# Performance work log

Measured on AMD Instinct MI355X. Metric: run time of the kernel, lower is better.

## Reference

```python
import jax, jax.numpy as jnp
import numpy as np

B, S, R, V, C, K, H = 256, 64, 256, 2000, 10, 6, 4
D = 256
DH = D // H
NEG = -1e9


def setup_inputs() -> dict:
    key = jax.random.key(0)
    ks = jax.random.split(key, 32)
    w = lambda i, shape: jax.random.normal(ks[i], shape, jnp.float32) * 0.05
    inp = {}
    inp["vis_emb"] = jax.random.normal(ks[0], (B * S, D), jnp.float32)
    # multi-hot concept vectors (sparse 0/1)
    inp["basic"] = (jax.random.uniform(ks[1], (R, V)) < 0.01).astype(jnp.float32)
    inp["crucial"] = (jax.random.uniform(ks[2], (R, V)) < 0.01).astype(jnp.float32)
    # to_b / to_k linears
    inp["Wtb"], inp["btb"] = w(3, (V, D)), w(4, (D,))
    inp["Wtk"], inp["btk"] = w(5, (V, D)), w(6, (D,))
    # cross attention (rule2vis): q/k/v/out projections
    inp["Wq"], inp["bq"] = w(7, (D, D)), w(8, (D,))
    inp["Wk"], inp["bk"] = w(9, (D, D)), w(10, (D,))
    inp["Wv"], inp["bv"] = w(11, (D, D)), w(12, (D,))
    inp["Wo"], inp["bo"] = w(13, (D, D)), w(14, (D,))
    # per-class GAT stacks: GAT(256->128), GAT(128->64), Linear(64->K)
    inp["W1"], inp["a1s"], inp["a1d"], inp["b1"] = w(15, (C, D, 128)), w(16, (C, 128)), w(17, (C, 128)), w(18, (C, 128))
    inp["W2"], inp["a2s"], inp["a2d"], inp["b2"] = w(19, (C, 128, 64)), w(20, (C, 64)), w(21, (C, 64)), w(22, (C, 64))
    inp["Wl"], inp["bl"] = w(23, (C, 64, K)), w(24, (C, K))
    # rule-graph adjacency: symmetric + self loops (PyG GATConv adds self loops)
    a0 = jax.random.uniform(ks[25], (R, R)) < 0.05
    inp["adj"] = a0 | a0.T | jnp.eye(R, dtype=bool)
    # class membership mask: each rule node belongs to one class head
    cls = jax.random.randint(ks[26], (R,), 0, C)
    inp["mask"] = (cls[None, :] == jnp.arange(C)[:, None]).astype(jnp.int32)
    return inp


def _gat(h, W, a_s, a_d, b, adj_bias):
    # h: [B,R,Fin] -> [B,R,Fout]; single-head PyG-style GATConv over dense adj
    hW = h @ W                                             # [B,R,F]
    e_dst = jnp.einsum('brf,f->br', hW, a_d)               # dst term
    e_src = jnp.einsum('brf,f->br', hW, a_s)               # src term
    e = jax.nn.leaky_relu(e_dst[:, :, None] + e_src[:, None, :], 0.2)  # [B,Rdst,Rsrc]
    alpha = jax.nn.softmax(e + adj_bias[None], axis=-1)
    return jnp.einsum('bij,bjf->bif', alpha, hW) + b


def reference(vis_emb, basic, crucial, Wtb, btb, Wtk, btk, Wq, bq, Wk, bk, Wv, bv,
              Wo, bo, W1, a1s, a1d, b1, W2, a2s, a2d, b2, Wl, bl, adj, mask):
    # rule embeddings: to_b(basic) + to_k(crucial)
    rule = basic @ Wtb + btb + crucial @ Wtk + btk         # [R,D]
    kv = vis_emb.reshape(B, S, D)
    q = jnp.broadcast_to(rule[None], (B, R, D))
    Q = (q @ Wq + bq).reshape(B, R, H, DH)
    Kx = (kv @ Wk + bk).reshape(B, S, H, DH)
    Vx = (kv @ Wv + bv).reshape(B, S, H, DH)
    att = jnp.einsum('brhd,bshd->bhrs', Q, Kx) / jnp.sqrt(jnp.float32(DH))
    att = jax.nn.softmax(att, axis=-1)
    emb = jnp.einsum('bhrs,bshd->brhd', att, Vx).reshape(B, R, D) @ Wo + bo  # [B,R,D]

    adj_bias = jnp.where(adj, 0.0, NEG).astype(emb.dtype)  # [R,R]
    outs = []
    for c in range(C):  # small fixed number of class heads
        h = emb * mask[c].astype(emb.dtype)[None, :, None]
        h = jax.nn.relu(_gat(h, W1[c], a1s[c], a1d[c], b1[c], adj_bias))
        h = _gat(h, W2[c], a2s[c], a2d[c], b2[c], adj_bias)  # dropout = eval identity
        h = h @ Wl[c] + bl[c]                                # [B,R,K]
        outs.append(jax.nn.log_softmax(h.sum(axis=1), axis=1))
    return jnp.stack(outs)  # [C,B,K]
```

## Files before the change

kernel.cpp:

```cpp
#include <hip/hip_runtime.h>
#include <stdint.h>

#define NB 256
#define NS 64
#define NR 256
#define NV 2000
#define NC 10
#define NK 6
#define ND 256

typedef __attribute__((ext_vector_type(8))) short bf16x8;
typedef __attribute__((ext_vector_type(4))) float f32x4;

__device__ __forceinline__ float bf2f(uint16_t u) {
  return __uint_as_float(((uint32_t)u) << 16);
}
__device__ __forceinline__ uint16_t f2bf(float f) {
  uint32_t x = __float_as_uint(f);
  x += 0x7FFFu + ((x >> 16) & 1u);
  return (uint16_t)(x >> 16);
}

__global__ __launch_bounds__(256) void k_front(
    const void* __restrict__ adj_raw, const int* __restrict__ mask,
    const float* __restrict__ W2, const float* __restrict__ a2s,
    const float* __restrict__ a2d,
    uint32_t* __restrict__ adjbits, int* __restrict__ cls,
    int* __restrict__ lists, int* __restrict__ cnt,
    int* __restrict__ deg, uint8_t* __restrict__ nbr,
    int8_t* __restrict__ midx,
    float* __restrict__ ud2, float* __restrict__ us2,
    const float* __restrict__ Wo, const float* __restrict__ Wk,
    const float* __restrict__ Wv, const float* __restrict__ W1,
    uint16_t* __restrict__ WOT, uint16_t* __restrict__ WKVT,
    uint16_t* __restrict__ W1T,
    const float* __restrict__ basic, const float* __restrict__ cruc,
    const float* __restrict__ Wtb, const float* __restrict__ btb,
    const float* __restrict__ Wtk, const float* __restrict__ btk,
    const float* __restrict__ Wq, const float* __restrict__ bq,
    uint16_t* __restrict__ Qbf,
    const float* __restrict__ vis, const float* __restrict__ bk,
    const float* __restrict__ bv,
    uint16_t* __restrict__ KX, uint16_t* __restrict__ VX)
{
  __shared__ char smem[33792];
  int bid = blockIdx.x;
  int tid = threadIdx.x;
  if (bid < 11) {
    if (bid == 0) {
      int* s_is4 = (int*)smem;
      if (tid == 0) *s_is4 = 1;
      __syncthreads();
      const uint32_t* u = (const uint32_t*)adj_raw;
      int ok = 1;
      for (int idx = tid; idx < 16384; idx += 256) {
        uint32_t v = u[idx];
        if (!(v == 0u || v == 1u || v == 0x3F800000u)) ok = 0;
      }
      if (!ok) atomicAnd(s_is4, 0);
      __syncthreads();
      int is4 = *s_is4;
      const uint8_t* b8 = (const uint8_t*)adj_raw;
      int dg = 0;
      for (int w = 0; w < 8; ++w) {
        uint32_t word = 0;
        for (int jb = 0; jb < 32; ++jb) {
          int j = w * 32 + jb;
          int bit = is4 ? (u[tid * 256 + j] != 0u) : (b8[tid * 256 + j] != 0);
          if (bit) {
            word |= (1u << jb);
            if (dg < 64) nbr[tid * 64 + dg] = (uint8_t)j;
            dg++;
          }
        }
        adjbits[tid * 8 + w] = word;
      }
      deg[tid] = (dg > 64) ? 64 : dg;
      int c = 0;
      for (int cc = 0; cc < NC; ++cc) if (mask[cc * 256 + tid] != 0) c = cc;
      cls[tid] = c;
      __syncthreads();
      if (tid == 0) {
        int cn[NC];
        for (int i = 0; i < NC; ++i) cn[i] = 0;
        for (int r = 0; r < 256; ++r) {
          int cc = cls[r];
          if (cn[cc] < 64) lists[cc * 64 + cn[cc]] = r;
          cn[cc]++;
        }
        for (int i = 0; i < NC; ++i) cnt[i] = (cn[i] > 64) ? 64 : cn[i];
        for (int i = 0; i < NC * 256; ++i) midx[i] = -1;
        for (int cc = 0; cc < NC; ++cc)
          for (int i = 0; i < cnt[cc]; ++i)
            midx[cc * 256 + lists[cc * 64 + i]] = (int8_t)i;
      }
    } else {
      int c = bid - 1;
      if (tid < 128) {
        float s1 = 0.f, s2 = 0.f;
        for (int g = 0; g < 64; ++g) {
          float w = W2[(c * 128 + tid) * 64 + g];
          s1 += w * a2d[c * 64 + g];
          s2 += w * a2s[c * 64 + g];
        }
        ud2[c * 128 + tid] = s1;
        us2[c * 128 + tid] = s2;
      }
    }
  } else if (bid < 139) {
    float (*ts)[65] = (float(*)[65])smem;
    int pb = bid - 11;
    const float* src;
    uint16_t* dst;
    int ncols, kt, nt;
    if (pb < 16)      { src = Wo; dst = WOT; ncols = 256; kt = pb >> 2; nt = pb & 3; }
    else if (pb < 32) { int t = pb - 16; src = Wk; dst = WKVT; ncols = 256; kt = t >> 2; nt = t & 3; }
    else if (pb < 48) { int t = pb - 32; src = Wv; dst = WKVT + 256 * 256; ncols = 256; kt = t >> 2; nt = t & 3; }
    else { int t = pb - 48; int c = t >> 3; int tt = t & 7;
           src = W1 + (long)c * 256 * 128; dst = W1T + (long)c * 128 * 256;
           ncols = 128; kt = tt >> 1; nt = tt & 1; }
    for (int idx = tid; idx < 4096; idx += 256) {
      int i = idx >> 6, j = idx & 63;
      ts[i][j] = src[(long)(kt * 64 + i) * ncols + nt * 64 + j];
    }
    __syncthreads();
    for (int idx = tid; idx < 4096; idx += 256) {
      int i = idx >> 6, j = idx & 63;
      dst[(long)(nt * 64 + i) * 256 + kt * 64 + j] = f2bf(ts[j][i]);
    }
  } else if (bid < 395) {
    float* row_s  = (float*)smem;
    float* rule_s = row_s + 2048;
    int*   nzi    = (int*)(rule_s + 256);
    float* nzv    = (float*)(nzi + 128);
    int*   nzcp   = (int*)(nzv + 128);
    int r = bid - 139;
    float acc = btb[tid] + btk[tid];
    for (int m = 0; m < 2; ++m) {
      const float* src = m ? cruc : basic;
      const float* W   = m ? Wtk : Wtb;
      for (int idx = tid; idx < 2048; idx += 256)
        row_s[idx] = (idx < NV) ? src[r * NV + idx] : 0.0f;
      if (tid == 0) *nzcp = 0;
      __syncthreads();
      if (tid < 64) {
        int base = 0;
        for (int ch = 0; ch < 32; ++ch) {
          int idx = ch * 64 + tid;
          float v = row_s[idx];
          unsigned long long bm = __ballot(v != 0.0f);
          if (v != 0.0f) {
            int pos = base + (int)__popcll(bm & ((1ull << tid) - 1ull));
            if (pos < 128) { nzi[pos] = idx; nzv[pos] = v; }
          }
          base += (int)__popcll(bm);
        }
        if (tid == 0) *nzcp = (base > 128) ? 128 : base;
      }
      __syncthreads();
      int n = *nzcp;
      for (int t = 0; t < n; ++t) acc += nzv[t] * W[nzi[t] * 256 + tid];
      __syncthreads();
    }
    rule_s[tid] = acc;
    __syncthreads();
    float q = bq[tid];
    for (int k2 = 0; k2 < 256; ++k2) q += rule_s[k2] * Wq[k2 * 256 + tid];
    Qbf[r * 256 + tid] = f2bf(q * 0.125f);
  } else {
    uint16_t* A_s = (uint16_t*)smem;
    int t = bid - 395;
    int bx = t & 255, by = t >> 8;
    int lane = tid & 63, w = tid >> 6;
    int r15 = lane & 15, kg = lane >> 4;
    long m0 = (long)bx * 64;
    int n0 = by * 64 + w * 16;
    for (int idx = tid; idx < 2048; idx += 256) {
      int r = idx >> 5, ch = idx & 31;
      const float4* p = (const float4*)&vis[(m0 + r) * 256 + ch * 8];
      float4 v0 = p[0], v1 = p[1];
      uint4 wd;
      wd.x = (uint32_t)f2bf(v0.x) | ((uint32_t)f2bf(v0.y) << 16);
      wd.y = (uint32_t)f2bf(v0.z) | ((uint32_t)f2bf(v0.w) << 16);
      wd.z = (uint32_t)f2bf(v1.x) | ((uint32_t)f2bf(v1.y) << 16);
      wd.w = (uint32_t)f2bf(v1.z) | ((uint32_t)f2bf(v1.w) << 16);
      *(uint4*)&A_s[r * 264 + ch * 8] = wd;
    }
    __syncthreads();
    const uint16_t* bptr = &WKVT[(long)(n0 + r15) * 256 + kg * 8];
    f32x4 acc[4];
    #pragma unroll
    for (int mt = 0; mt < 4; ++mt) acc[mt] = (f32x4){0.f, 0.f, 0.f, 0.f};
    #pragma unroll
    for (int ks = 0; ks < 8; ++ks) {
      bf16x8 bfr = *(const bf16x8*)(bptr + ks * 32);
      #pragma unroll
      for (int mt = 0; mt < 4; ++mt) {
        bf16x8 afr = *(const bf16x8*)&A_s[(mt * 16 + r15) * 264 + kg * 8 + ks * 32];
        acc[mt] = __builtin_amdgcn_mfma_f32_16x16x32_bf16(afr, bfr, acc[mt], 0, 0, 0);
      }
    }
    int col = n0 + r15;
    float bb = (col < 256) ? bk[col] : bv[col - 256];
    uint16_t* outp = (col < 256) ? KX : VX;
    int oc = (col < 256) ? col : col - 256;
    #pragma unroll
    for (int mt = 0; mt < 4; ++mt)
      #pragma unroll
      for (int j = 0; j < 4; ++j) {
        long row = m0 + mt * 16 + kg * 4 + j;
        outp[row * 256 + oc] = f2bf(acc[mt][j] + bb);
      }
  }
}

__global__ __launch_bounds__(512) void k_attn(const uint16_t* __restrict__ Qbf,
                         const uint16_t* __restrict__ KX, const uint16_t* __restrict__ VX,
                         uint16_t* __restrict__ EMB)
{
  __shared__ uint16_t p_s[128 * 72];
  __shared__ uint16_t vt_s[64 * 72];
  int tid = threadIdx.x;
  int lane = tid & 63, w = tid >> 6;
  int r15 = lane & 15, kg = lane >> 4;
  int b = blockIdx.x >> 1;
  int rbase = (blockIdx.x & 1) * 128;
  for (int h = 0; h < 4; ++h) {
    __syncthreads();
    for (int idx = tid; idx < 2048; idx += 512) {
      int s = idx >> 5, d2 = (idx & 31) * 2;
      uint32_t v = *(const uint32_t*)&VX[((long)(b * 64 + s)) * 256 + h * 64 + d2];
      vt_s[d2 * 72 + s] = (uint16_t)(v & 0xffff);
      vt_s[(d2 + 1) * 72 + s] = (uint16_t)(v >> 16);
    }
    __syncthreads();
    f32x4 sacc[4];
    #pragma unroll
    for (int nt = 0; nt < 4; ++nt) sacc[nt] = (f32x4){0.f, 0.f, 0.f, 0.f};
    #pragma unroll
    for (int ks = 0; ks < 2; ++ks) {
      bf16x8 afr = *(const bf16x8*)&Qbf[(long)(rbase + w * 16 + r15) * 256 + h * 64 + ks * 32 + kg * 8];
      #pragma unroll
      for (int nt = 0; nt < 4; ++nt) {
        bf16x8 bfr = *(const bf16x8*)&KX[((long)(b * 64 + nt * 16 + r15)) * 256 + h * 64 + ks * 32 + kg * 8];
        sacc[nt] = __builtin_amdgcn_mfma_f32_16x16x32_bf16(afr, bfr, sacc[nt], 0, 0, 0);
      }
    }
    #pragma unroll
    for (int j = 0; j < 4; ++j) {
      float m = sacc[0][j];
      #pragma unroll
      for (int nt = 1; nt < 4; ++nt) m = fmaxf(m, sacc[nt][j]);
      m = fmaxf(m, __shfl_xor(m, 1));
      m = fmaxf(m, __shfl_xor(m, 2));
      m = fmaxf(m, __shfl_xor(m, 4));
      m = fmaxf(m, __shfl_xor(m, 8));
      float pv[4];
      float sum = 0.f;
      #pragma unroll
      for (int nt = 0; nt < 4; ++nt) { pv[nt] = __expf(sacc[nt][j] - m); sum += pv[nt]; }
      sum += __shfl_xor(sum, 1);
      sum += __shfl_xor(sum, 2);
      sum += __shfl_xor(sum, 4);
      sum += __shfl_xor(sum, 8);
      float rs = 1.0f / sum;
      #pragma unroll
      for (int nt = 0; nt < 4; ++nt)
        p_s[(w * 16 + kg * 4 + j) * 72 + nt * 16 + r15] = f2bf(pv[nt] * rs);
    }
    f32x4 oacc[4];
    #pragma unroll
    for (int nt = 0; nt < 4; ++nt) oacc[nt] = (f32x4){0.f, 0.f, 0.f, 0.f};
    #pragma unroll
    for (int ks = 0; ks < 2; ++ks) {
      bf16x8 afr = *(const bf16x8*)&p_s[(w * 16 + r15) * 72 + ks * 32 + kg * 8];
      #pragma unroll
      for (int nt = 0; nt < 4; ++nt) {
        bf16x8 bfr = *(const bf16x8*)&vt_s[(nt * 16 + r15) * 72 + ks * 32 + kg * 8];
        oacc[nt] = __builtin_amdgcn_mfma_f32_16x16x32_bf16(afr, bfr, oacc[nt], 0, 0, 0);
      }
    }
    #pragma unroll
    for (int nt = 0; nt < 4; ++nt)
      #pragma unroll
      for (int j = 0; j < 4; ++j) {
        long row = (long)(b * 256 + rbase + w * 16 + kg * 4 + j);
        EMB[row * 256 + h * 64 + nt * 16 + r15] = f2bf(oacc[nt][j]);
      }
  }
}

__global__ __launch_bounds__(256) void k_wo(uint16_t* __restrict__ EMB,
                    const uint16_t* __restrict__ WOT, const float* __restrict__ bo)
{
  __shared__ uint16_t A_s[64 * 264];
  int tid = threadIdx.x;
  int lane = tid & 63, w = tid >> 6;
  int r15 = lane & 15, kg = lane >> 4;
  long m0 = (long)blockIdx.x * 64;
  for (int idx = tid; idx < 2048; idx += 256) {
    int r = idx >> 5, ch = idx & 31;
    uint4 v = *(const uint4*)&EMB[(m0 + r) * 256 + ch * 8];
    *(uint4*)&A_s[r * 264 + ch * 8] = v;
  }
  __syncthreads();
  #pragma unroll
  for (int nt = 0; nt < 4; ++nt) {
    int n0 = nt * 64 + w * 16;
    const uint16_t* bptr = &WOT[(long)(n0 + r15) * 256 + kg * 8];
    f32x4 acc[4];
    #pragma unroll
    for (int mt = 0; mt < 4; ++mt) acc[mt] = (f32x4){0.f, 0.f, 0.f, 0.f};
    #pragma unroll
    for (int ks = 0; ks < 8; ++ks) {
      bf16x8 bfr = *(const bf16x8*)(bptr + ks * 32);
      #pragma unroll
      for (int mt = 0; mt < 4; ++mt) {
        bf16x8 afr = *(const bf16x8*)&A_s[(mt * 16 + r15) * 264 + kg * 8 + ks * 32];
        acc[mt] = __builtin_amdgcn_mfma_f32_16x16x32_bf16(afr, bfr, acc[mt], 0, 0, 0);
      }
    }
    int col = n0 + r15;
    float bb = bo[col];
    #pragma unroll
    for (int mt = 0; mt < 4; ++mt)
      #pragma unroll
      for (int j = 0; j < 4; ++j) {
        long row = m0 + mt * 16 + kg * 4 + j;
        EMB[row * 256 + col] = f2bf(acc[mt][j] + bb);
      }
  }
}

__global__ __launch_bounds__(1024) void k_gat(
    const uint16_t* __restrict__ EMB, const uint16_t* __restrict__ W1T,
    const float* __restrict__ a1d, const float* __restrict__ a1s,
    const int* __restrict__ lists, const int* __restrict__ cnt_g,
    const int* __restrict__ deg_g, const uint8_t* __restrict__ nbr_g,
    const int8_t* __restrict__ midx_g,
    const float* __restrict__ b1, const float* __restrict__ ud2_g,
    const float* __restrict__ us2_g, const float* __restrict__ W2,
    const float* __restrict__ b2, const float* __restrict__ Wl,
    const float* __restrict__ bl, float* __restrict__ out)
{
  __shared__ uint16_t alphaA[256 * 72], alphaB[256 * 72];
  __shared__ uint16_t hwtA[128 * 72], hwtB[128 * 72];
  __shared__ float e1dA_s[256], e1sA_s[256], e1dB_s[256], e1sB_s[256];
  __shared__ float rd1A_s[256], rd1B_s[256];
  __shared__ float e2dA_s[256], e2sA_s[256], e2dB_s[256], e2sB_s[256];
  __shared__ float rd2A_s[256], rd2B_s[256];
  __shared__ float a1d_s[128], a1s_s[128], b1_s[128], ud2_s[128], us2_s[128];
  __shared__ float t_sA[128], t_sB[128];
  __shared__ int   list_s[64];
  __shared__ int8_t midx_s[256];
  float (*tpartA)[128] = (float(*)[128])alphaA;
  float (*tpartB)[128] = (float(*)[128])alphaB;
  float* wjA_s = rd1A_s;
  float* wjB_s = rd1B_s;
  float* svecA = (float*)hwtA;
  float* lvecA = (float*)(hwtA + 256);
  float* svecB = (float*)hwtB;
  float* lvecB = (float*)(hwtB + 256);
  int tid = threadIdx.x;
  int lane = tid & 63, w = tid >> 6;
  int r15 = lane & 15, kg = lane >> 4;
  int c = blockIdx.x >> 7, bp = blockIdx.x & 127;
  int bA = bp * 2, bB = bp * 2 + 1;
  int n = cnt_g[c];
  if (tid < 64) list_s[tid] = (tid < n) ? lists[c * 64 + tid] : 0;
  if (tid >= 64 && tid < 128) {
    int i = tid - 64;
    ((uint32_t*)midx_s)[i] = ((const uint32_t*)(midx_g + (long)c * 256))[i];
  }
  if (tid < 128) {
    a1d_s[tid] = a1d[c * 128 + tid];
    a1s_s[tid] = a1s[c * 128 + tid];
    b1_s[tid]  = b1[c * 128 + tid];
    ud2_s[tid] = ud2_g[c * 128 + tid];
    us2_s[tid] = us2_g[c * 128 + tid];
  }
  if (tid < 256) {
    e1dA_s[tid] = 0.f; e1sA_s[tid] = 0.f;
    e1dB_s[tid] = 0.f; e1sB_s[tid] = 0.f;
  }
  int r = tid >> 2, q = tid & 3;
  int dg = deg_g[r];
  int t0 = q * 16;
  int ncnt = dg - t0; ncnt = (ncnt < 0) ? 0 : (ncnt > 16 ? 16 : ncnt);
  const uint32_t* np = (const uint32_t*)&nbr_g[r * 64 + t0];
  uint32_t nbw0 = np[0], nbw1 = np[1], nbw2 = np[2], nbw3 = np[3];
  __syncthreads();
  int mt = w & 3, nh = w >> 2;
  int colA = nh * 32 + r15, colB = colA + 16;
  const uint16_t* bptr = &W1T[((long)c * 128 + colA) * 256 + kg * 8];
  const uint16_t* arA = &EMB[((long)bA * 256 + list_s[mt * 16 + r15]) * 256 + kg * 8];
  const uint16_t* arB = &EMB[((long)bB * 256 + list_s[mt * 16 + r15]) * 256 + kg * 8];
  f32x4 aA0 = (f32x4){0.f,0.f,0.f,0.f}, aA1 = (f32x4){0.f,0.f,0.f,0.f};
  f32x4 aB0 = (f32x4){0.f,0.f,0.f,0.f}, aB1 = (f32x4){0.f,0.f,0.f,0.f};
  if (mt * 16 < n) {
    #pragma unroll
    for (int ks = 0; ks < 8; ++ks) {
      bf16x8 b0 = *(const bf16x8*)(bptr + ks * 32);
      bf16x8 b1f = *(const bf16x8*)(bptr + 16 * 256 + ks * 32);
      bf16x8 afA = *(const bf16x8*)(arA + ks * 32);
      bf16x8 afB = *(const bf16x8*)(arB + ks * 32);
      aA0 = __builtin_amdgcn_mfma_f32_16x16x32_bf16(afA, b0, aA0, 0, 0, 0);
      aA1 = __builtin_amdgcn_mfma_f32_16x16x32_bf16(afA, b1f, aA1, 0, 0, 0);
      aB0 = __builtin_amdgcn_mfma_f32_16x16x32_bf16(afB, b0, aB0, 0, 0, 0);
      aB1 = __builtin_amdgcn_mfma_f32_16x16x32_bf16(afB, b1f, aB1, 0, 0, 0);
    }
  }
  {
    uint2 pk;
    pk.x = (uint32_t)f2bf(aA0[0]) | ((uint32_t)f2bf(aA0[1]) << 16);
    pk.y = (uint32_t)f2bf(aA0[2]) | ((uint32_t)f2bf(aA0[3]) << 16);
    *(uint2*)&hwtA[colA * 72 + mt * 16 + kg * 4] = pk;
    pk.x = (uint32_t)f2bf(aA1[0]) | ((uint32_t)f2bf(aA1[1]) << 16);
    pk.y = (uint32_t)f2bf(aA1[2]) | ((uint32_t)f2bf(aA1[3]) << 16);
    *(uint2*)&hwtA[colB * 72 + mt * 16 + kg * 4] = pk;
    pk.x = (uint32_t)f2bf(aB0[0]) | ((uint32_t)f2bf(aB0[1]) << 16);
    pk.y = (uint32_t)f2bf(aB0[2]) | ((uint32_t)f2bf(aB0[3]) << 16);
    *(uint2*)&hwtB[colA * 72 + mt * 16 + kg * 4] = pk;
    pk.x = (uint32_t)f2bf(aB1[0]) | ((uint32_t)f2bf(aB1[1]) << 16);
    pk.y = (uint32_t)f2bf(aB1[2]) | ((uint32_t)f2bf(aB1[3]) << 16);
    *(uint2*)&hwtB[colB * 72 + mt * 16 + kg * 4] = pk;
    float adA = a1d_s[colA], adB = a1d_s[colB];
    float asA = a1s_s[colA], asB = a1s_s[colB];
    #pragma unroll
    for (int j = 0; j < 4; ++j) {
      float pdA = aA0[j] * adA + aA1[j] * adB;
      float psA = aA0[j] * asA + aA1[j] * asB;
      float pdB = aB0[j] * adA + aB1[j] * adB;
      float psB = aB0[j] * asA + aB1[j] * asB;
      pdA += __shfl_xor(pdA, 1); pdA += __shfl_xor(pdA, 2);
      pdA += __shfl_xor(pdA, 4); pdA += __shfl_xor(pdA, 8);
      psA += __shfl_xor(psA, 1); psA += __shfl_xor(psA, 2);
      psA += __shfl_xor(psA, 4); psA += __shfl_xor(psA, 8);
      pdB += __shfl_xor(pdB, 1); pdB += __shfl_xor(pdB, 2);
      pdB += __shfl_xor(pdB, 4); pdB += __shfl_xor(pdB, 8);
      psB += __shfl_xor(psB, 1); psB += __shfl_xor(psB, 2);
      psB += __shfl_xor(psB, 4); psB += __shfl_xor(psB, 8);
      if (r15 == 0) {
        int jm = mt * 16 + kg * 4 + j;
        e2dA_s[nh * 64 + jm] = pdA;
        e2sA_s[nh * 64 + jm] = psA;
        e2dB_s[nh * 64 + jm] = pdB;
        e2sB_s[nh * 64 + jm] = psB;
      }
    }
  }
  __syncthreads();
  {
    uint32_t* zA = (uint32_t*)&alphaA[r * 72 + q * 18];
    uint32_t* zB = (uint32_t*)&alphaB[r * 72 + q * 18];
    #pragma unroll
    for (int i = 0; i < 9; ++i) { zA[i] = 0u; zB[i] = 0u; }
  }
  if (tid < 64 && tid < n) {
    float sdA = e2dA_s[tid] + e2dA_s[tid + 64] + e2dA_s[tid + 128] + e2dA_s[tid + 192];
    float ssA = e2sA_s[tid] + e2sA_s[tid + 64] + e2sA_s[tid + 128] + e2sA_s[tid + 192];
    float sdB = e2dB_s[tid] + e2dB_s[tid + 64] + e2dB_s[tid + 128] + e2dB_s[tid + 192];
    float ssB = e2sB_s[tid] + e2sB_s[tid + 64] + e2sB_s[tid + 128] + e2sB_s[tid + 192];
    int rr = list_s[tid];
    e1dA_s[rr] = sdA; e1sA_s[rr] = ssA;
    e1dB_s[rr] = sdB; e1sB_s[rr] = ssB;
  }
  __syncthreads();
  {
    float e1dAv = e1dA_s[r], e1dBv = e1dB_s[r];
    float denA = 0.f, denB = 0.f;
    #define NB_CHUNK(WORD, BASE)                                            \
      _Pragma("unroll")                                                     \
      for (int ii = 0; ii < 4; ++ii) {                                      \
        if (BASE + ii < ncnt) {                                             \
          int j = (int)((WORD >> (ii * 8)) & 255u);                         \
          float eA = e1dAv + e1sA_s[j];                                     \
          eA = fmaxf(eA, 0.2f * eA); eA = fminf(eA, 60.f);                  \
          float wA = __expf(eA); denA += wA;                                \
          float eB = e1dBv + e1sB_s[j];                                     \
          eB = fmaxf(eB, 0.2f * eB); eB = fminf(eB, 60.f);                  \
          float wB = __expf(eB); denB += wB;                                \
          int mi = midx_s[j];                                               \
          if (mi >= 0) {                                                    \
            alphaA[r * 72 + mi] = f2bf(wA);                                 \
            alphaB[r * 72 + mi] = f2bf(wB);                                 \
          }                                                                 \
        }                                                                   \
      }
    NB_CHUNK(nbw0, 0) NB_CHUNK(nbw1, 4) NB_CHUNK(nbw2, 8) NB_CHUNK(nbw3, 12)
    #undef NB_CHUNK
    denA += __shfl_xor(denA, 1); denA += __shfl_xor(denA, 2);
    denB += __shfl_xor(denB, 1); denB += __shfl_xor(denB, 2);
    if (q == 0) { rd1A_s[r] = 1.0f / denA; rd1B_s[r] = 1.0f / denB; }
  }
  __syncthreads();
  f32x4 gA[8], gB[8];
  #pragma unroll
  for (int nt = 0; nt < 8; ++nt) {
    gA[nt] = (f32x4){0.f, 0.f, 0.f, 0.f};
    gB[nt] = (f32x4){0.f, 0.f, 0.f, 0.f};
  }
  int kslices = (n > 32) ? 2 : 1;
  for (int ks = 0; ks < kslices; ++ks) {
    bf16x8 afA = *(const bf16x8*)&alphaA[(w * 16 + r15) * 72 + ks * 32 + kg * 8];
    bf16x8 afB = *(const bf16x8*)&alphaB[(w * 16 + r15) * 72 + ks * 32 + kg * 8];
    #pragma unroll
    for (int nt = 0; nt < 8; ++nt) {
      bf16x8 bfA = *(const bf16x8*)&hwtA[(nt * 16 + r15) * 72 + ks * 32 + kg * 8];
      bf16x8 bfB = *(const bf16x8*)&hwtB[(nt * 16 + r15) * 72 + ks * 32 + kg * 8];
      gA[nt] = __builtin_amdgcn_mfma_f32_16x16x32_bf16(afA, bfA, gA[nt], 0, 0, 0);
      gB[nt] = __builtin_amdgcn_mfma_f32_16x16x32_bf16(afB, bfB, gB[nt], 0, 0, 0);
    }
  }
  {
    float rdA[4], rdB[4];
    #pragma unroll
    for (int j = 0; j < 4; ++j) {
      rdA[j] = rd1A_s[w * 16 + kg * 4 + j];
      rdB[j] = rd1B_s[w * 16 + kg * 4 + j];
    }
    float edA[4] = {0.f,0.f,0.f,0.f}, esA[4] = {0.f,0.f,0.f,0.f};
    float edB[4] = {0.f,0.f,0.f,0.f}, esB[4] = {0.f,0.f,0.f,0.f};
    #pragma unroll
    for (int nt = 0; nt < 8; ++nt) {
      float uf = ud2_s[nt * 16 + r15], sf = us2_s[nt * 16 + r15];
      float bf = b1_s[nt * 16 + r15];
      #pragma unroll
      for (int j = 0; j < 4; ++j) {
        float gvA = fmaxf(gA[nt][j] * rdA[j] + bf, 0.f);
        gA[nt][j] = gvA;
        edA[j] += gvA * uf; esA[j] += gvA * sf;
        float gvB = fmaxf(gB[nt][j] * rdB[j] + bf, 0.f);
        gB[nt][j] = gvB;
        edB[j] += gvB * uf; esB[j] += gvB * sf;
      }
    }
    #pragma unroll
    for (int j = 0; j < 4; ++j) {
      edA[j] += __shfl_xor(edA[j], 1); edA[j] += __shfl_xor(edA[j], 2);
      edA[j] += __shfl_xor(edA[j], 4); edA[j] += __shfl_xor(edA[j], 8);
      esA[j] += __shfl_xor(esA[j], 1); esA[j] += __shfl_xor(esA[j], 2);
      esA[j] += __shfl_xor(esA[j], 4); esA[j] += __shfl_xor(esA[j], 8);
      edB[j] += __shfl_xor(edB[j], 1); edB[j] += __shfl_xor(edB[j], 2);
      edB[j] += __shfl_xor(edB[j], 4); edB[j] += __shfl_xor(edB[j], 8);
      esB[j] += __shfl_xor(esB[j], 1); esB[j] += __shfl_xor(esB[j], 2);
      esB[j] += __shfl_xor(esB[j], 4); esB[j] += __shfl_xor(esB[j], 8);
      if (r15 == 0) {
        int rr = w * 16 + kg * 4 + j;
        e2dA_s[rr] = edA[j]; e2sA_s[rr] = esA[j];
        e2dB_s[rr] = edB[j]; e2sB_s[rr] = esB[j];
      }
    }
  }
  __syncthreads();
  {
    float e2dAv = e2dA_s[r], e2dBv = e2dB_s[r];
    float dnA = 0.f, dnB = 0.f;
    #define NB_CHUNK(WORD, BASE)                                            \
      _Pragma("unroll")                                                     \
      for (int ii = 0; ii < 4; ++ii) {                                      \
        if (BASE + ii < ncnt) {                                             \
          int j = (int)((WORD >> (ii * 8)) & 255u);                         \
          float eA = e2dAv + e2sA_s[j];                                     \
          eA = fmaxf(eA, 0.2f * eA); eA = fminf(eA, 60.f);                  \
          dnA += __expf(eA);                                                \
          float eB = e2dBv + e2sB_s[j];                                     \
          eB = fmaxf(eB, 0.2f * eB); eB = fminf(eB, 60.f);                  \
          dnB += __expf(eB);                                                \
        }                                                                   \
      }
    NB_CHUNK(nbw0, 0) NB_CHUNK(nbw1, 4) NB_CHUNK(nbw2, 8) NB_CHUNK(nbw3, 12)
    #undef NB_CHUNK
    dnA += __shfl_xor(dnA, 1); dnA += __shfl_xor(dnA, 2);
    dnB += __shfl_xor(dnB, 1); dnB += __shfl_xor(dnB, 2);
    if (q == 0) { rd2A_s[r] = 1.0f / dnA; rd2B_s[r] = 1.0f / dnB; }
  }
  __syncthreads();
  {
    float e2sAv = e2sA_s[r], e2sBv = e2sB_s[r];
    float wjA = 0.f, wjB = 0.f;
    #define NB_CHUNK(WORD, BASE)                                            \
      _Pragma("unroll")                                                     \
      for (int ii = 0; ii < 4; ++ii) {                                      \
        if (BASE + ii < ncnt) {                                             \
          int i2 = (int)((WORD >> (ii * 8)) & 255u);                        \
          float eA = e2dA_s[i2] + e2sAv;                                    \
          eA = fmaxf(eA, 0.2f * eA); eA = fminf(eA, 60.f);                  \
          wjA += __expf(eA) * rd2A_s[i2];                                   \
          float eB = e2dB_s[i2] + e2sBv;                                    \
          eB = fmaxf(eB, 0.2f * eB); eB = fminf(eB, 60.f);                  \
          wjB += __expf(eB) * rd2B_s[i2];                                   \
        }                                                                   \
      }
    NB_CHUNK(nbw0, 0) NB_CHUNK(nbw1, 4) NB_CHUNK(nbw2, 8) NB_CHUNK(nbw3, 12)
    #undef NB_CHUNK
    wjA += __shfl_xor(wjA, 1); wjA += __shfl_xor(wjA, 2);
    wjB += __shfl_xor(wjB, 1); wjB += __shfl_xor(wjB, 2);
    if (q == 0) { wjA_s[r] = wjA; wjB_s[r] = wjB; }
  }
  __syncthreads();
  {
    float wvA[4], wvB[4];
    #pragma unroll
    for (int j = 0; j < 4; ++j) {
      wvA[j] = wjA_s[w * 16 + kg * 4 + j];
      wvB[j] = wjB_s[w * 16 + kg * 4 + j];
    }
    #pragma unroll
    for (int nt = 0; nt < 8; ++nt) {
      float tpA = wvA[0]*gA[nt][0] + wvA[1]*gA[nt][1] + wvA[2]*gA[nt][2] + wvA[3]*gA[nt][3];
      float tpB = wvB[0]*gB[nt][0] + wvB[1]*gB[nt][1] + wvB[2]*gB[nt][2] + wvB[3]*gB[nt][3];
      tpA += __shfl_xor(tpA, 16); tpA += __shfl_xor(tpA, 32);
      tpB += __shfl_xor(tpB, 16); tpB += __shfl_xor(tpB, 32);
      if (kg == 0) {
        tpartA[w][nt * 16 + r15] = tpA;
        tpartB[w][nt * 16 + r15] = tpB;
      }
    }
  }
  __syncthreads();
  if (tid < 128) {
    float s = 0.f;
    #pragma unroll
    for (int w2 = 0; w2 < 16; ++w2) s += tpartA[w2][tid];
    t_sA[tid] = s;
  } else if (tid < 256) {
    int f = tid - 128;
    float s = 0.f;
    #pragma unroll
    for (int w2 = 0; w2 < 16; ++w2) s += tpartB[w2][f];
    t_sB[f] = s;
  }
  __syncthreads();
  {
    int batch = tid >> 9;
    int tt = tid & 511;
    int col = tt & 63, fg = tt >> 6;
    const float* tsrc = batch ? t_sB : t_sA;
    float sp = 0.f;
    #pragma unroll
    for (int i = 0; i < 16; ++i) {
      int f = fg * 16 + i;
      sp += tsrc[f] * W2[((long)c * 128 + f) * 64 + col];
    }
    if (batch) tpartB[fg][col] = sp; else tpartA[fg][col] = sp;
  }
  __syncthreads();
  if (tid < 64) {
    float s = 256.0f * b2[c * 64 + tid];
    #pragma unroll
    for (int fg = 0; fg < 8; ++fg) s += tpartA[fg][tid];
    svecA[tid] = s;
  } else if (tid >= 512 && tid < 576) {
    int col = tid - 512;
    float s = 256.0f * b2[c * 64 + col];
    #pragma unroll
    for (int fg = 0; fg < 8; ++fg) s += tpartB[fg][col];
    svecB[col] = s;
  }
  __syncthreads();
  if (tid < 6) {
    float lg = 256.0f * bl[c * 6 + tid];
    for (int f = 0; f < 64; ++f) lg += svecA[f] * Wl[((long)c * 64 + f) * 6 + tid];
    lvecA[tid] = lg;
  } else if (tid >= 512 && tid < 518) {
    int k = tid - 512;
    float lg = 256.0f * bl[c * 6 + k];
    for (int f = 0; f < 64; ++f) lg += svecB[f] * Wl[((long)c * 64 + f) * 6 + k];
    lvecB[k] = lg;
  }
  __syncthreads();
  if (tid == 0) {
    float mm = lvecA[0];
    for (int k2 = 1; k2 < 6; ++k2) mm = fmaxf(mm, lvecA[k2]);
    float ss = 0.f;
    for (int k2 = 0; k2 < 6; ++k2) ss += __expf(lvecA[k2] - mm);
    float lse = mm + __logf(ss);
    for (int k2 = 0; k2 < 6; ++k2) out[((long)c * 256 + bA) * 6 + k2] = lvecA[k2] - lse;
  } else if (tid == 512) {
    float mm = lvecB[0];
    for (int k2 = 1; k2 < 6; ++k2) mm = fmaxf(mm, lvecB[k2]);
    float ss = 0.f;
    for (int k2 = 0; k2 < 6; ++k2) ss += __expf(lvecB[k2] - mm);
    float lse = mm + __logf(ss);
    for (int k2 = 0; k2 < 6; ++k2) out[((long)c * 256 + bB) * 6 + k2] = lvecB[k2] - lse;
  }
}

extern "C" void kernel_launch(void* const* d_in, const int* in_sizes, int n_in,
                              void* d_out, int out_size, void* d_ws, size_t ws_size,
                              hipStream_t stream)
{
  const float* vis   = (const float*)d_in[0];
  const float* basic = (const float*)d_in[1];
  const float* cruc  = (const float*)d_in[2];
  const float* Wtb   = (const float*)d_in[3];
  const float* btb   = (const float*)d_in[4];
  const float* Wtk   = (const float*)d_in[5];
  const float* btk   = (const float*)d_in[6];
  const float* Wq    = (const float*)d_in[7];
  const float* bq    = (const float*)d_in[8];
  const float* Wk    = (const float*)d_in[9];
  const float* bk    = (const float*)d_in[10];
  const float* Wv    = (const float*)d_in[11];
  const float* bv    = (const float*)d_in[12];
  const float* Wo    = (const float*)d_in[13];
  const float* bo    = (const float*)d_in[14];
  const float* W1    = (const float*)d_in[15];
  const float* a1s   = (const float*)d_in[16];
  const float* a1d   = (const float*)d_in[17];
  const float* b1    = (const float*)d_in[18];
  const float* W2    = (const float*)d_in[19];
  const float* a2s   = (const float*)d_in[20];
  const float* a2d   = (const float*)d_in[21];
  const float* b2    = (const float*)d_in[22];
  const float* Wl    = (const float*)d_in[23];
  const float* bl    = (const float*)d_in[24];
  const void*  adj   = d_in[25];
  const int*   mask  = (const int*)d_in[26];
  float* out = (float*)d_out;
  char* ws = (char*)d_ws;

  uint16_t* QBF  = (uint16_t*)(ws + 0);
  uint32_t* ADJ  = (uint32_t*)(ws + 262144);
  int*      CLS  = (int*)(ws + 270336);
  int*      LST  = (int*)(ws + 271360);
  int*      CNT  = (int*)(ws + 273920);
  int*      DEG  = (int*)(ws + 273984);
  uint8_t*  NBR  = (uint8_t*)(ws + 275008);
  int8_t*   MIDX = (int8_t*)(ws + 291392);
  float*    UD2  = (float*)(ws + 293952);
  float*    US2  = (float*)(ws + 299072);
  uint16_t* WOT  = (uint16_t*)(ws + 304192);
  uint16_t* WKVT = (uint16_t*)(ws + 435264);
  uint16_t* W1T  = (uint16_t*)(ws + 697408);
  uint16_t* KX   = (uint16_t*)(ws + 1352768);
  uint16_t* VX   = (uint16_t*)(ws + 9741376);
  uint16_t* EMB  = (uint16_t*)(ws + 18129984);

  hipLaunchKernelGGL(k_front, dim3(2443), dim3(256), 0, stream,
                     adj, mask, W2, a2s, a2d, ADJ, CLS, LST, CNT, DEG, NBR, MIDX,
                     UD2, US2,
                     Wo, Wk, Wv, W1, WOT, WKVT, W1T,
                     basic, cruc, Wtb, btb, Wtk, btk, Wq, bq, QBF,
                     vis, bk, bv, KX, VX);
  hipLaunchKernelGGL(k_attn, dim3(512), dim3(512), 0, stream, QBF, KX, VX, EMB);
  hipLaunchKernelGGL(k_wo, dim3(1024), dim3(256), 0, stream, EMB, WOT, bo);
  hipLaunchKernelGGL(k_gat, dim3(1280), dim3(1024), 0, stream,
                     EMB, W1T, a1d, a1s, LST, CNT, DEG, NBR, MIDX,
                     b1, UD2, US2, W2, b2, Wl, bl, out);
}
```

Baseline: 361.0 us.

## Fold Wo projection into per-class W1 weights and drop k_wo kernel

Precomputes Wo·W1[c] per class (as bf16 FT) and bo·W1[c] as a per-class bias inside the front kernel, so the GAT first-layer matmul reads the raw attention output directly. This removes the separate k_wo kernel, including its full read and write of the EMB tensor and one launch. It adds a small weight-weight GEMM to the front kernel and changes rounding, since the product is rounded to bf16 once instead of rounding the intermediate embedding.

```diff
diff --git a/kernel.cpp b/kernel.cpp
--- a/kernel.cpp
+++ b/kernel.cpp
@@ -32,8 +32,9 @@
     float* __restrict__ ud2, float* __restrict__ us2,
     const float* __restrict__ Wo, const float* __restrict__ Wk,
     const float* __restrict__ Wv, const float* __restrict__ W1,
-    uint16_t* __restrict__ WOT, uint16_t* __restrict__ WKVT,
-    uint16_t* __restrict__ W1T,
+    const float* __restrict__ bo,
+    uint16_t* __restrict__ WKVT, uint16_t* __restrict__ FT,
+    float* __restrict__ BW1,
     const float* __restrict__ basic, const float* __restrict__ cruc,
     const float* __restrict__ Wtb, const float* __restrict__ btb,
     const float* __restrict__ Wtk, const float* __restrict__ btk,
@@ -105,36 +106,83 @@
         }
         ud2[c * 128 + tid] = s1;
         us2[c * 128 + tid] = s2;
-      }
-    }
-  } else if (bid < 139) {
+        float s3 = 0.f;
+        for (int m = 0; m < 256; ++m)
+          s3 += bo[m] * W1[(long)c * 32768 + m * 128 + tid];
+        BW1[c * 128 + tid] = s3;
+      }
+    }
+  } else if (bid < 43) {
     float (*ts)[65] = (float(*)[65])smem;
     int pb = bid - 11;
     const float* src;
     uint16_t* dst;
-    int ncols, kt, nt;
-    if (pb < 16)      { src = Wo; dst = WOT; ncols = 256; kt = pb >> 2; nt = pb & 3; }
-    else if (pb < 32) { int t = pb - 16; src = Wk; dst = WKVT; ncols = 256; kt = t >> 2; nt = t & 3; }
-    else if (pb < 48) { int t = pb - 32; src = Wv; dst = WKVT + 256 * 256; ncols = 256; kt = t >> 2; nt = t & 3; }
-    else { int t = pb - 48; int c = t >> 3; int tt = t & 7;
-           src = W1 + (long)c * 256 * 128; dst = W1T + (long)c * 128 * 256;
-           ncols = 128; kt = tt >> 1; nt = tt & 1; }
+    int kt, nt;
+    if (pb < 16)      { src = Wk; dst = WKVT; kt = pb >> 2; nt = pb & 3; }
+    else { int t = pb - 16; src = Wv; dst = WKVT + 256 * 256; kt = t >> 2; nt = t & 3; }
     for (int idx = tid; idx < 4096; idx += 256) {
       int i = idx >> 6, j = idx & 63;
-      ts[i][j] = src[(long)(kt * 64 + i) * ncols + nt * 64 + j];
+      ts[i][j] = src[(long)(kt * 64 + i) * 256 + nt * 64 + j];
     }
     __syncthreads();
     for (int idx = tid; idx < 4096; idx += 256) {
       int i = idx >> 6, j = idx & 63;
       dst[(long)(nt * 64 + i) * 256 + kt * 64 + j] = f2bf(ts[j][i]);
     }
-  } else if (bid < 395) {
+  } else if (bid < 83) {
+    uint16_t* ts = (uint16_t*)smem;
+    int pb = bid - 43;
+    int c = pb >> 2, mt = pb & 3;
+    int lane = tid & 63, w = tid >> 6;
+    int r15 = lane & 15, kg = lane >> 4;
+    int k0 = mt * 64;
+    int colA = w * 32 + r15, colB = colA + 16;
+    f32x4 acc[4][2];
+    #pragma unroll
+    for (int m2 = 0; m2 < 4; ++m2) {
+      acc[m2][0] = (f32x4){0.f, 0.f, 0.f, 0.f};
+      acc[m2][1] = (f32x4){0.f, 0.f, 0.f, 0.f};
+    }
+    for (int s4 = 0; s4 < 4; ++s4) {
+      __syncthreads();
+      for (int idx = tid; idx < 8192; idx += 256) {
+        int i = idx >> 7, nn = idx & 127;
+        ts[nn * 72 + i] = f2bf(W1[(long)c * 32768 + (s4 * 64 + i) * 128 + nn]);
+      }
+      __syncthreads();
+      #pragma unroll
+      for (int kk = 0; kk < 2; ++kk) {
+        bf16x8 bA = *(const bf16x8*)&ts[colA * 72 + kk * 32 + kg * 8];
+        bf16x8 bB = *(const bf16x8*)&ts[colB * 72 + kk * 32 + kg * 8];
+        #pragma unroll
+        for (int m2 = 0; m2 < 4; ++m2) {
+          const float* wp = &Wo[(long)(k0 + m2 * 16 + r15) * 256 + s4 * 64 + kk * 32 + kg * 8];
+          float4 f0 = *(const float4*)wp, f1 = *(const float4*)(wp + 4);
+          union { bf16x8 v; uint32_t u[4]; } af;
+          af.u[0] = (uint32_t)f2bf(f0.x) | ((uint32_t)f2bf(f0.y) << 16);
+          af.u[1] = (uint32_t)f2bf(f0.z) | ((uint32_t)f2bf(f0.w) << 16);
+          af.u[2] = (uint32_t)f2bf(f1.x) | ((uint32_t)f2bf(f1.y) << 16);
+          af.u[3] = (uint32_t)f2bf(f1.z) | ((uint32_t)f2bf(f1.w) << 16);
+          acc[m2][0] = __builtin_amdgcn_mfma_f32_16x16x32_bf16(af.v, bA, acc[m2][0], 0, 0, 0);
+          acc[m2][1] = __builtin_amdgcn_mfma_f32_16x16x32_bf16(af.v, bB, acc[m2][1], 0, 0, 0);
+        }
+      }
+    }
+    #pragma unroll
+    for (int m2 = 0; m2 < 4; ++m2)
+      #pragma unroll
+      for (int j = 0; j < 4; ++j) {
+        int k = k0 + m2 * 16 + kg * 4 + j;
+        FT[(long)c * 32768 + colA * 256 + k] = f2bf(acc[m2][0][j]);
+        FT[(long)c * 32768 + colB * 256 + k] = f2bf(acc[m2][1][j]);
+      }
+  } else if (bid < 339) {
     float* row_s  = (float*)smem;
     float* rule_s = row_s + 2048;
     int*   nzi    = (int*)(rule_s + 256);
     float* nzv    = (float*)(nzi + 128);
     int*   nzcp   = (int*)(nzv + 128);
-    int r = bid - 139;
+    int r = bid - 83;
     float acc = btb[tid] + btk[tid];
     for (int m = 0; m < 2; ++m) {
       const float* src = m ? cruc : basic;
@@ -169,7 +217,7 @@
     Qbf[r * 256 + tid] = f2bf(q * 0.125f);
   } else {
     uint16_t* A_s = (uint16_t*)smem;
-    int t = bid - 395;
+    int t = bid - 339;
     int bx = t & 255, by = t >> 8;
     int lane = tid & 63, w = tid >> 6;
     int r15 = lane & 15, kg = lane >> 4;
@@ -290,50 +338,9 @@
   }
 }
 
-__global__ __launch_bounds__(256) void k_wo(uint16_t* __restrict__ EMB,
-                    const uint16_t* __restrict__ WOT, const float* __restrict__ bo)
-{
-  __shared__ uint16_t A_s[64 * 264];
-  int tid = threadIdx.x;
-  int lane = tid & 63, w = tid >> 6;
-  int r15 = lane & 15, kg = lane >> 4;
-  long m0 = (long)blockIdx.x * 64;
-  for (int idx = tid; idx < 2048; idx += 256) {
-    int r = idx >> 5, ch = idx & 31;
-    uint4 v = *(const uint4*)&EMB[(m0 + r) * 256 + ch * 8];
-    *(uint4*)&A_s[r * 264 + ch * 8] = v;
-  }
-  __syncthreads();
-  #pragma unroll
-  for (int nt = 0; nt < 4; ++nt) {
-    int n0 = nt * 64 + w * 16;
-    const uint16_t* bptr = &WOT[(long)(n0 + r15) * 256 + kg * 8];
-    f32x4 acc[4];
-    #pragma unroll
-    for (int mt = 0; mt < 4; ++mt) acc[mt] = (f32x4){0.f, 0.f, 0.f, 0.f};
-    #pragma unroll
-    for (int ks = 0; ks < 8; ++ks) {
-      bf16x8 bfr = *(const bf16x8*)(bptr + ks * 32);
-      #pragma unroll
-      for (int mt = 0; mt < 4; ++mt) {
-        bf16x8 afr = *(const bf16x8*)&A_s[(mt * 16 + r15) * 264 + kg * 8 + ks * 32];
-        acc[mt] = __builtin_amdgcn_mfma_f32_16x16x32_bf16(afr, bfr, acc[mt], 0, 0, 0);
-      }
-    }
-    int col = n0 + r15;
-    float bb = bo[col];
-    #pragma unroll
-    for (int mt = 0; mt < 4; ++mt)
-      #pragma unroll
-      for (int j = 0; j < 4; ++j) {
-        long row = m0 + mt * 16 + kg * 4 + j;
-        EMB[row * 256 + col] = f2bf(acc[mt][j] + bb);
-      }
-  }
-}
-
 __global__ __launch_bounds__(1024) void k_gat(
-    const uint16_t* __restrict__ EMB, const uint16_t* __restrict__ W1T,
+    const uint16_t* __restrict__ EMB, const uint16_t* __restrict__ FT,
+    const float* __restrict__ BW1,
     const float* __restrict__ a1d, const float* __restrict__ a1s,
     const int* __restrict__ lists, const int* __restrict__ cnt_g,
     const int* __restrict__ deg_g, const uint8_t* __restrict__ nbr_g,
@@ -350,6 +357,7 @@
   __shared__ float e2dA_s[256], e2sA_s[256], e2dB_s[256], e2sB_s[256];
   __shared__ float rd2A_s[256], rd2B_s[256];
   __shared__ float a1d_s[128], a1s_s[128], b1_s[128], ud2_s[128], us2_s[128];
+  __shared__ float bw1_s[128];
   __shared__ float t_sA[128], t_sB[128];
   __shared__ int   list_s[64];
   __shared__ int8_t midx_s[256];
@@ -378,6 +386,7 @@
     b1_s[tid]  = b1[c * 128 + tid];
     ud2_s[tid] = ud2_g[c * 128 + tid];
     us2_s[tid] = us2_g[c * 128 + tid];
+    bw1_s[tid] = BW1[c * 128 + tid];
   }
   if (tid < 256) {
     e1dA_s[tid] = 0.f; e1sA_s[tid] = 0.f;
@@ -392,7 +401,7 @@
   __syncthreads();
   int mt = w & 3, nh = w >> 2;
   int colA = nh * 32 + r15, colB = colA + 16;
-  const uint16_t* bptr = &W1T[((long)c * 128 + colA) * 256 + kg * 8];
+  const uint16_t* bptr = &FT[((long)c * 128 + colA) * 256 + kg * 8];
   const uint16_t* arA = &EMB[((long)bA * 256 + list_s[mt * 16 + r15]) * 256 + kg * 8];
   const uint16_t* arB = &EMB[((long)bB * 256 + list_s[mt * 16 + r15]) * 256 + kg * 8];
   f32x4 aA0 = (f32x4){0.f,0.f,0.f,0.f}, aA1 = (f32x4){0.f,0.f,0.f,0.f};
@@ -411,6 +420,12 @@
     }
   }
   {
+    float bwA = bw1_s[colA], bwB = bw1_s[colB];
+    #pragma unroll
+    for (int j = 0; j < 4; ++j) {
+      aA0[j] += bwA; aA1[j] += bwB;
+      aB0[j] += bwA; aB1[j] += bwB;
+    }
     uint2 pk;
     pk.x = (uint32_t)f2bf(aA0[0]) | ((uint32_t)f2bf(aA0[1]) << 16);
     pk.y = (uint32_t)f2bf(aA0[2]) | ((uint32_t)f2bf(aA0[3]) << 16);
@@ -731,22 +746,21 @@
   int8_t*   MIDX = (int8_t*)(ws + 291392);
   float*    UD2  = (float*)(ws + 293952);
   float*    US2  = (float*)(ws + 299072);
-  uint16_t* WOT  = (uint16_t*)(ws + 304192);
+  float*    BW1  = (float*)(ws + 304192);
   uint16_t* WKVT = (uint16_t*)(ws + 435264);
-  uint16_t* W1T  = (uint16_t*)(ws + 697408);
+  uint16_t* FT   = (uint16_t*)(ws + 697408);
   uint16_t* KX   = (uint16_t*)(ws + 1352768);
   uint16_t* VX   = (uint16_t*)(ws + 9741376);
   uint16_t* EMB  = (uint16_t*)(ws + 18129984);
 
-  hipLaunchKernelGGL(k_front, dim3(2443), dim3(256), 0, stream,
+  hipLaunchKernelGGL(k_front, dim3(2387), dim3(256), 0, stream,
                      adj, mask, W2, a2s, a2d, ADJ, CLS, LST, CNT, DEG, NBR, MIDX,
                      UD2, US2,
-                     Wo, Wk, Wv, W1, WOT, WKVT, W1T,
+                     Wo, Wk, Wv, W1, bo, WKVT, FT, BW1,
                      basic, cruc, Wtb, btb, Wtk, btk, Wq, bq, QBF,
                      vis, bk, bv, KX, VX);
   hipLaunchKernelGGL(k_attn, dim3(512), dim3(512), 0, stream, QBF, KX, VX, EMB);
-  hipLaunchKernelGGL(k_wo, dim3(1024), dim3(256), 0, stream, EMB, WOT, bo);
   hipLaunchKernelGGL(k_gat, dim3(1280), dim3(1024), 0, stream,
-                     EMB, W1T, a1d, a1s, LST, CNT, DEG, NBR, MIDX,
+                     EMB, FT, BW1, a1d, a1s, LST, CNT, DEG, NBR, MIDX,
                      b1, UD2, US2, W2, b2, Wl, bl, out);
 }
```

After: 338.5 us. -6.2%, faster.
